# Optimization experiments

Hardware: AMD Instinct MI355X
Metric: run time of the kernel (lower is better)

## Reference

```python
import jax, jax.numpy as jnp
import numpy as np

B, N, C = 2, 8192, 64      # batch, points, feature channels
M = 2048                    # FPS-sampled centers (num_point)
KS = (16, 32)               # KNN sizes per scale
H, O = 128, 128             # EGNN hidden / output channels
S = len(KS)


def setup_inputs() -> dict:
    key = jax.random.key(0)
    k = jax.random.split(key, 12)
    sc = 0.05
    return {
        "points_xyz": jax.random.normal(k[0], (B, N, 3), jnp.float32),
        "features":   jax.random.normal(k[1], (B, C, N), jnp.float32),
        # edge MLP phi_e: [h_i, h_j, ||x_i-x_j||^2] -> H -> H
        "we1": jax.random.normal(k[2], (S, 2 * C + 1, H)) * sc,
        "be1": jnp.zeros((S, H)),
        "we2": jax.random.normal(k[3], (S, H, H)) * sc,
        "be2": jnp.zeros((S, H)),
        # coord MLP phi_x: H -> 1
        "wx": jax.random.normal(k[4], (S, H, 1)) * sc,
        "bx": jnp.zeros((S, 1)),
        # node MLP phi_h: [h_i, sum_j m_ij] -> H -> O
        "wh1": jax.random.normal(k[5], (S, C + H, H)) * sc,
        "bh1": jnp.zeros((S, H)),
        "wh2": jax.random.normal(k[6], (S, H, O)) * sc,
        "bh2": jnp.zeros((S, O)),
    }


def fps(xyz, m):
    """D-FPS: farthest point sampling by Euclidean distance. xyz (B,N,3) -> idx (B,m) int32."""
    b, n, _ = xyz.shape
    start = jnp.zeros((b,), jnp.int32)
    mind0 = jnp.full((b, n), 1e10, xyz.dtype)

    def step(carry, _):
        mind, last = carry
        lxyz = jnp.take_along_axis(xyz, last[:, None, None], axis=1)  # (B,1,3)
        d = jnp.sum((xyz - lxyz) ** 2, axis=-1)                       # (B,N)
        mind = jnp.minimum(mind, d)
        nxt = jnp.argmax(mind, axis=1).astype(jnp.int32)
        return (mind, nxt), nxt

    (_, _), rest = jax.lax.scan(step, (mind0, start), None, length=m - 1)
    return jnp.concatenate([start[:, None], rest.T], axis=1)  # (B,m)


def _forward(points_xyz, features, we1, be1, we2, be2, wx, bx, wh1, bh1, wh2, bh2):
    idx = fps(points_xyz, M)                                           # (B,M)
    dsamp_xyz = jnp.take_along_axis(points_xyz, idx[:, :, None], axis=1)   # (B,M,3)
    dsamp_feat = jnp.take_along_axis(features, idx[:, None, :], axis=2)    # (B,C,M)
    h_i = dsamp_feat.transpose(0, 2, 1)                                # (B,M,C)

    # pairwise squared distances centers->all points (B,M,N)
    d2 = (jnp.sum(dsamp_xyz ** 2, -1)[:, :, None]
          + jnp.sum(points_xyz ** 2, -1)[:, None, :]
          - 2.0 * jnp.einsum('bmd,bnd->bmn', dsamp_xyz, points_xyz))

    shifted, feats = [], []
    for i, k in enumerate(KS):
        _, nidx = jax.lax.top_k(-d2, k)                                # (B,M,k) KNN indices
        neigh_xyz = jax.vmap(lambda p, ii: p[ii])(points_xyz, nidx)    # (B,M,k,3)
        neigh_feat = jax.vmap(lambda f, ii: f[:, ii])(features, nidx)  # (B,C,M,k)
        h_j = neigh_feat.transpose(0, 2, 3, 1)                         # (B,M,k,C)

        rel = dsamp_xyz[:, :, None, :] - neigh_xyz                     # (B,M,k,3)
        dist2 = jnp.sum(rel * rel, -1, keepdims=True)                  # (B,M,k,1)

        e_in = jnp.concatenate(
            [jnp.broadcast_to(h_i[:, :, None, :], h_j.shape), h_j, dist2], axis=-1)
        m_ij = jax.nn.silu(e_in @ we1[i] + be1[i])
        m_ij = jax.nn.silu(m_ij @ we2[i] + be2[i])                     # (B,M,k,H)

        coef = m_ij @ wx[i] + bx[i]                                    # (B,M,k,1)
        x_shift = dsamp_xyz + jnp.mean(rel * coef, axis=2)             # (B,M,3)

        agg = jnp.sum(m_ij, axis=2)                                    # (B,M,H)
        h_out = jax.nn.silu(jnp.concatenate([h_i, agg], -1) @ wh1[i] + bh1[i]) @ wh2[i] + bh2[i]

        shifted.append(x_shift)
        feats.append(h_out.transpose(0, 2, 1))                         # (B,O,M)

    return (dsamp_xyz,
            jnp.concatenate(shifted, axis=1),    # (B, S*M, 3)
            jnp.concatenate(feats, axis=1),      # (B, S*O, M)
            idx)


def reference(points_xyz, features, we1, be1, we2, be2, wx, bx, wh1, bh1, wh2, bh2):
    return _forward(points_xyz, features, we1, be1, we2, be2, wx, bx, wh1, bh1, wh2, bh2)
```

## Files before the change

kernel.cpp:

```cpp
#include <hip/hip_runtime.h>
#include <stdint.h>
#include <math.h>

#define NPTS  8192
#define NB    2
#define NC    64
#define MCENT 2048
#define HH    128
#define K2NN  32

#define OUT0_OFF 0
#define OUT1_OFF (NB*MCENT*3)
#define OUT2_OFF (OUT1_OFF + NB*2*MCENT*3)
#define OUT3_OFF (OUT2_OFF + NB*2*HH*MCENT)

__device__ __forceinline__ float silu_f(float v){ return v / (1.0f + expf(-v)); }

template<int CTRL>
__device__ __forceinline__ unsigned dppmov(unsigned v){
  return (unsigned)__builtin_amdgcn_update_dpp(0, (int)v, CTRL, 0xF, 0xF, true);
}
__device__ __forceinline__ unsigned wave_max_u32(unsigned v){
  unsigned s;
  s = dppmov<0xB1>(v);  v = v > s ? v : s;
  s = dppmov<0x4E>(v);  v = v > s ? v : s;
  s = dppmov<0x141>(v); v = v > s ? v : s;
  s = dppmov<0x140>(v); v = v > s ? v : s;
  s = (unsigned)__builtin_amdgcn_ds_swizzle((int)v, 0x401F); v = v > s ? v : s;
  s = (unsigned)__shfl_xor((int)v, 32); v = v > s ? v : s;
  return v;
}
__device__ __forceinline__ unsigned wave_min_u32(unsigned v){
  unsigned s;
  s = dppmov<0xB1>(v);  v = v < s ? v : s;
  s = dppmov<0x4E>(v);  v = v < s ? v : s;
  s = dppmov<0x141>(v); v = v < s ? v : s;
  s = dppmov<0x140>(v); v = v < s ? v : s;
  s = (unsigned)__builtin_amdgcn_ds_swizzle((int)v, 0x401F); v = v < s ? v : s;
  s = (unsigned)__shfl_xor((int)v, 32); v = v < s ? v : s;
  return v;
}

__global__ __launch_bounds__(512, 2) void fps_kernel(const float* __restrict__ xyz,
                                                     float* __restrict__ out,
                                                     int* __restrict__ ws_idx){
#pragma clang fp contract(off)
  __shared__ float xs[NPTS], ys[NPTS], zs[NPTS];
  __shared__ unsigned long long warr[2][8];
  const int b   = blockIdx.x;
  const int tid = threadIdx.x;
  const float* P = xyz + (size_t)b * NPTS * 3;

  float x[16], y[16], z[16], mind[16];
  #pragma unroll
  for (int j = 0; j < 16; ++j){
    const int p = tid*16 + j;
    const float px = P[p*3+0], py = P[p*3+1], pz = P[p*3+2];
    x[j] = px; y[j] = py; z[j] = pz; mind[j] = 1e10f;
    xs[p] = px; ys[p] = py; zs[p] = pz;
  }
  float cx = P[0], cy = P[1], cz = P[2];
  if (tid == 0){
    ws_idx[b*MCENT] = 0;
    out[OUT3_OFF + b*MCENT] = 0.0f;
    out[OUT0_OFF + (size_t)(b*MCENT)*3 + 0] = cx;
    out[OUT0_OFF + (size_t)(b*MCENT)*3 + 1] = cy;
    out[OUT0_OFF + (size_t)(b*MCENT)*3 + 2] = cz;
  }
  __syncthreads();

  for (int t = 1; t < MCENT; ++t){
    float bestv = -1.0f; int bestp = tid*16;
    #pragma unroll
    for (int j = 0; j < 16; ++j){
      const float dx = x[j]-cx, dy = y[j]-cy, dz = z[j]-cz;
      const float d  = (dx*dx + dy*dy) + dz*dz;
      const float mn = fminf(mind[j], d);
      mind[j] = mn;
      if (mn > bestv){ bestv = mn; bestp = tid*16 + j; }
    }
    const unsigned vb = __float_as_uint(bestv);
    const unsigned wv = wave_max_u32(vb);
    const unsigned long long bal = __ballot(vb == wv);
    const int lane = __ffsll(bal) - 1;
    const int wp   = __shfl(bestp, lane);
    if ((tid & 63) == 0)
      warr[t & 1][tid >> 6] = ((unsigned long long)wv << 32) | (unsigned)(NPTS-1-wp);
    __syncthreads();
    unsigned long long kb = warr[t & 1][0];
    #pragma unroll
    for (int w = 1; w < 8; ++w){
      const unsigned long long k2 = warr[t & 1][w];
      if (k2 > kb) kb = k2;
    }
    const int p = NPTS - 1 - (int)(kb & 0xFFFFFFFFULL);
    cx = xs[p]; cy = ys[p]; cz = zs[p];
    if (tid == 0){
      ws_idx[b*MCENT + t] = p;
      out[OUT3_OFF + b*MCENT + t] = (float)p;
      out[OUT0_OFF + (size_t)(b*MCENT + t)*3 + 0] = cx;
      out[OUT0_OFF + (size_t)(b*MCENT + t)*3 + 1] = cy;
      out[OUT0_OFF + (size_t)(b*MCENT + t)*3 + 2] = cz;
    }
  }
}

__global__ __launch_bounds__(256) void knn_kernel(const float* __restrict__ xyz,
                                                  const float* __restrict__ out,
                                                  int* __restrict__ ws_knn){
#pragma clang fp contract(off)
  __shared__ unsigned d2u[NPTS];
  __shared__ unsigned long long warr[2][4];
  const int blk = blockIdx.x;
  const int b = blk / MCENT, m = blk % MCENT;
  const int tid = threadIdx.x;
  const float* P = xyz + (size_t)b*NPTS*3;
  const float cx = out[OUT0_OFF + (size_t)(b*MCENT+m)*3 + 0];
  const float cy = out[OUT0_OFF + (size_t)(b*MCENT+m)*3 + 1];
  const float cz = out[OUT0_OFF + (size_t)(b*MCENT+m)*3 + 2];
  const float cn = (cx*cx + cy*cy) + cz*cz;

  unsigned long long best = ~0ULL, second = ~0ULL;
  #pragma unroll 4
  for (int j = 0; j < NPTS/256; ++j){
    const int p = tid + 256*j;
    const float px = P[p*3+0], py = P[p*3+1], pz = P[p*3+2];
    const float pn = (px*px + py*py) + pz*pz;
    const float e  = (cx*px + cy*py) + cz*pz;
    const float d2 = (cn + pn) - 2.0f*e;
    unsigned u = __float_as_uint(d2);
    u = (u & 0x80000000u) ? ~u : (u | 0x80000000u);
    d2u[p] = u;
    const unsigned long long kk = ((unsigned long long)u << 32) | (unsigned)p;
    if      (kk < best)  { second = best; best = kk; }
    else if (kk < second){ second = kk; }
  }
  __syncthreads();

  for (int it = 0; it < K2NN; ++it){
    const unsigned vb = (unsigned)(best >> 32);
    const unsigned wv = wave_min_u32(vb);
    const unsigned long long bal = __ballot(vb == wv);
    unsigned long long k;
    if (__popcll(bal) == 1){
      const int lane = __ffsll(bal) - 1;
      const unsigned lp = (unsigned)__shfl((int)(unsigned)best, lane);
      k = ((unsigned long long)wv << 32) | lp;
    } else {
      k = best;
      #pragma unroll
      for (int o = 32; o > 0; o >>= 1){
        const unsigned long long k2 = __shfl_xor(k, o);
        if (k2 < k) k = k2;
      }
    }
    if ((tid & 63) == 0) warr[it & 1][tid >> 6] = k;
    __syncthreads();
    unsigned long long kb = warr[it & 1][0];
    #pragma unroll
    for (int w = 1; w < 4; ++w){
      const unsigned long long k2 = warr[it & 1][w];
      if (k2 < kb) kb = k2;
    }
    const unsigned p = (unsigned)kb;
    if (tid == 0) ws_knn[(size_t)blk*K2NN + it] = (int)p;
    if (best == kb){
      d2u[p] = 0xFFFFFFFFu;
      best = second; second = ~0ULL;
      if (best == ~0ULL){
        #pragma unroll 4
        for (int j = 0; j < NPTS/256; ++j){
          const int q = tid + 256*j;
          const unsigned long long kk = ((unsigned long long)d2u[q] << 32) | (unsigned)q;
          if      (kk < best)  { second = best; best = kk; }
          else if (kk < second){ second = kk; }
        }
      }
    }
  }
}

#define S1STR 132

template<int KNB>
__device__ __forceinline__ void egnn_scale(
    int isc, int b, int m, int tid,
    const float* __restrict__ we1, const float* __restrict__ be1,
    const float* __restrict__ we2, const float* __restrict__ be2,
    const float* __restrict__ wxw, const float* __restrict__ bxw,
    const float* __restrict__ wh1, const float* __restrict__ bh1,
    const float* __restrict__ wh2, const float* __restrict__ bh2,
    const float* hi, const float (*hj)[NC], const float (*rel)[3],
    const float* d2s, float (*s1)[S1STR], float (*s2)[S1STR],
    float* coefs, float* aggs, float* t1,
    float cx, float cy, float cz, float* __restrict__ out)
{
  constexpr int KH = KNB/2;
  const int h  = tid & 127;
  const int jg = tid >> 7;
  const int j0 = jg * KH;
  const float* W1 = we1 + (size_t)isc*129*HH;
  const float* W2 = we2 + (size_t)isc*HH*HH;

  float shi = be1[isc*HH + h];
  for (int r = 0; r < NC; ++r) shi += hi[r] * W1[r*HH + h];
  float acc[KH];
  #pragma unroll
  for (int jl = 0; jl < KH; ++jl) acc[jl] = shi;
  for (int r4 = 0; r4 < NC/4; ++r4){
    const float w0 = W1[(NC + 4*r4+0)*HH + h];
    const float w1 = W1[(NC + 4*r4+1)*HH + h];
    const float w2 = W1[(NC + 4*r4+2)*HH + h];
    const float w3 = W1[(NC + 4*r4+3)*HH + h];
    #pragma unroll
    for (int jl = 0; jl < KH; ++jl){
      const float4 v = *(const float4*)&hj[j0+jl][4*r4];
      acc[jl] += v.x*w0; acc[jl] += v.y*w1; acc[jl] += v.z*w2; acc[jl] += v.w*w3;
    }
  }
  {
    const float wd = W1[128*HH + h];
    #pragma unroll
    for (int jl = 0; jl < KH; ++jl)
      s1[j0+jl][h] = silu_f(acc[jl] + d2s[j0+jl]*wd);
  }
  __syncthreads();

  float acc2[KH];
  {
    const float b2 = be2[isc*HH + h];
    #pragma unroll
    for (int jl = 0; jl < KH; ++jl) acc2[jl] = b2;
  }
  for (int r4 = 0; r4 < HH/4; ++r4){
    const float w0 = W2[(4*r4+0)*HH + h];
    const float w1 = W2[(4*r4+1)*HH + h];
    const float w2 = W2[(4*r4+2)*HH + h];
    const float w3 = W2[(4*r4+3)*HH + h];
    #pragma unroll
    for (int jl = 0; jl < KH; ++jl){
      const float4 v = *(const float4*)&s1[j0+jl][4*r4];
      acc2[jl] += v.x*w0; acc2[jl] += v.y*w1; acc2[jl] += v.z*w2; acc2[jl] += v.w*w3;
    }
  }
  #pragma unroll
  for (int jl = 0; jl < KH; ++jl)
    s2[j0+jl][h] = silu_f(acc2[jl]);
  __syncthreads();

  if (tid < HH){
    float a = 0.f;
    #pragma unroll
    for (int j = 0; j < KNB; ++j) a += s2[j][tid];
    aggs[tid] = a;
  } else if (tid < HH + KNB){
    const int j = tid - HH;
    const float* WX = wxw + isc*HH;
    float c = 0.f;
    for (int r = 0; r < HH; ++r) c += s2[j][r]*WX[r];
    coefs[j] = c + bxw[isc];
  }
  __syncthreads();

  if (tid < 3){
    float s = 0.f;
    #pragma unroll
    for (int j = 0; j < KNB; ++j) s += rel[j][tid]*coefs[j];
    const float cc = (tid==0) ? cx : ((tid==1) ? cy : cz);
    out[OUT1_OFF + ((size_t)(b*2 + isc)*MCENT + m)*3 + tid] = cc + s*(1.0f/KNB);
  }

  if (tid < HH){
    const float* WH1 = wh1 + (size_t)isc*(NC+HH)*HH;
    float n = bh1[isc*HH + tid];
    for (int r = 0; r < NC; ++r) n += hi[r]*WH1[r*HH + tid];
    for (int r = 0; r < HH; ++r) n += aggs[r]*WH1[(NC+r)*HH + tid];
    t1[tid] = silu_f(n);
  }
  __syncthreads();

  if (tid < HH){
    const float* WH2 = wh2 + (size_t)isc*HH*HH;
    float v = bh2[isc*HH + tid];
    for (int r = 0; r < HH; ++r) v += t1[r]*WH2[r*HH + tid];
    out[OUT2_OFF + ((size_t)(b*2*HH) + isc*HH + tid)*MCENT + m] = v;
  }
  __syncthreads();
}

__global__ __launch_bounds__(256) void egnn_kernel(
    const float* __restrict__ xyz,  const float* __restrict__ feat,
    const float* __restrict__ we1,  const float* __restrict__ be1,
    const float* __restrict__ we2,  const float* __restrict__ be2,
    const float* __restrict__ wxw,  const float* __restrict__ bxw,
    const float* __restrict__ wh1,  const float* __restrict__ bh1,
    const float* __restrict__ wh2,  const float* __restrict__ bh2,
    const int* __restrict__ ws_idx, const int* __restrict__ ws_knn,
    float* __restrict__ out)
{
  __shared__ __align__(16) float hi[NC];
  __shared__ __align__(16) float hj[K2NN][NC];
  __shared__ float rel[K2NN][3];
  __shared__ float d2s[K2NN];
  __shared__ __align__(16) float s1[K2NN][S1STR];
  __shared__ __align__(16) float s2[K2NN][S1STR];
  __shared__ float coefs[K2NN];
  __shared__ float aggs[HH];
  __shared__ float t1[HH];
  __shared__ int   nidx[K2NN];

  const int blk = blockIdx.x;
  const int b = blk / MCENT, m = blk % MCENT;
  const int tid = threadIdx.x;
  const float* P = xyz + (size_t)b*NPTS*3;
  const float cx = out[OUT0_OFF + (size_t)(b*MCENT+m)*3 + 0];
  const float cy = out[OUT0_OFF + (size_t)(b*MCENT+m)*3 + 1];
  const float cz = out[OUT0_OFF + (size_t)(b*MCENT+m)*3 + 2];

  const int ci = ws_idx[b*MCENT + m];
  if (tid < NC)   hi[tid]   = feat[((size_t)b*NC + tid)*NPTS + ci];
  if (tid < K2NN) nidx[tid] = ws_knn[(size_t)blk*K2NN + tid];
  __syncthreads();

  if (tid < K2NN){
    const int p = nidx[tid];
    const float rx = cx - P[p*3+0];
    const float ry = cy - P[p*3+1];
    const float rz = cz - P[p*3+2];
    rel[tid][0]=rx; rel[tid][1]=ry; rel[tid][2]=rz;
    d2s[tid] = rx*rx + ry*ry + rz*rz;
  }
  {
    const int j  = tid >> 3;
    const int c0 = (tid & 7) * 8;
    const int p  = nidx[j];
    #pragma unroll
    for (int q = 0; q < 8; ++q)
      hj[j][c0+q] = feat[((size_t)b*NC + c0 + q)*NPTS + p];
  }
  __syncthreads();

  egnn_scale<16>(0, b, m, tid, we1, be1, we2, be2, wxw, bxw, wh1, bh1, wh2, bh2,
                 hi, hj, rel, d2s, s1, s2, coefs, aggs, t1, cx, cy, cz, out);
  egnn_scale<32>(1, b, m, tid, we1, be1, we2, be2, wxw, bxw, wh1, bh1, wh2, bh2,
                 hi, hj, rel, d2s, s1, s2, coefs, aggs, t1, cx, cy, cz, out);
}

extern "C" void kernel_launch(void* const* d_in, const int* in_sizes, int n_in,
                              void* d_out, int out_size, void* d_ws, size_t ws_size,
                              hipStream_t stream){
  const float* xyz = (const float*)d_in[0];
  const float* feat= (const float*)d_in[1];
  const float* we1 = (const float*)d_in[2];
  const float* be1 = (const float*)d_in[3];
  const float* we2 = (const float*)d_in[4];
  const float* be2 = (const float*)d_in[5];
  const float* wxw = (const float*)d_in[6];
  const float* bxw = (const float*)d_in[7];
  const float* wh1 = (const float*)d_in[8];
  const float* bh1 = (const float*)d_in[9];
  const float* wh2 = (const float*)d_in[10];
  const float* bh2 = (const float*)d_in[11];
  float* out = (float*)d_out;

  int* ws_idx = (int*)d_ws;
  int* ws_knn = ws_idx + NB*MCENT;

  fps_kernel <<<dim3(NB),        dim3(512), 0, stream>>>(xyz, out, ws_idx);
  knn_kernel <<<dim3(NB*MCENT),  dim3(256), 0, stream>>>(xyz, out, ws_knn);
  egnn_kernel<<<dim3(NB*MCENT),  dim3(256), 0, stream>>>(xyz, feat,
      we1, be1, we2, be2, wxw, bxw, wh1, bh1, wh2, bh2, ws_idx, ws_knn, out);
}
```

Before: 2.388 ms.

## Fuse FPS, KNN and EGNN into one persistent kernel with progress flags

```diff
diff --git a/kernel.cpp b/kernel.cpp
--- a/kernel.cpp
+++ b/kernel.cpp
@@ -8,27 +8,38 @@
 #define MCENT 2048
 #define HH    128
 #define K2NN  32
+#define S1STR 132
+#define GRID  256
+#define PUBMASK 7
 
 #define OUT0_OFF 0
 #define OUT1_OFF (NB*MCENT*3)
 #define OUT2_OFF (OUT1_OFF + NB*2*MCENT*3)
 #define OUT3_OFF (OUT2_OFF + NB*2*HH*MCENT)
 
+#define SM_SIZE  98432
+#define SM_XS    0
+#define SM_YS    32768
+#define SM_ZS    65536
+#define SM_FWARR 98304
+#define SM_D2U   0
+#define SM_S1    0
+#define SM_S2    16896
+#define SM_HJ    33792
+#define SM_HI    41984
+#define SM_REL   42240
+#define SM_D2S   42624
+#define SM_AGG   42752
+#define SM_T1    43264
+#define SM_COEF  43776
+#define SM_NIDX  43904
+#define SM_CWARR 44032
+
 __device__ __forceinline__ float silu_f(float v){ return v / (1.0f + expf(-v)); }
 
 template<int CTRL>
 __device__ __forceinline__ unsigned dppmov(unsigned v){
   return (unsigned)__builtin_amdgcn_update_dpp(0, (int)v, CTRL, 0xF, 0xF, true);
-}
-__device__ __forceinline__ unsigned wave_max_u32(unsigned v){
-  unsigned s;
-  s = dppmov<0xB1>(v);  v = v > s ? v : s;
-  s = dppmov<0x4E>(v);  v = v > s ? v : s;
-  s = dppmov<0x141>(v); v = v > s ? v : s;
-  s = dppmov<0x140>(v); v = v > s ? v : s;
-  s = (unsigned)__builtin_amdgcn_ds_swizzle((int)v, 0x401F); v = v > s ? v : s;
-  s = (unsigned)__shfl_xor((int)v, 32); v = v > s ? v : s;
-  return v;
 }
 __device__ __forceinline__ unsigned wave_min_u32(unsigned v){
   unsigned s;
@@ -41,14 +52,18 @@
   return v;
 }
 
-__global__ __launch_bounds__(512, 2) void fps_kernel(const float* __restrict__ xyz,
-                                                     float* __restrict__ out,
-                                                     int* __restrict__ ws_idx){
+__device__ void fps_block(const int b, const int tid,
+                          const float* __restrict__ xyz,
+                          float* __restrict__ out,
+                          int* __restrict__ ws_idx,
+                          int* __restrict__ prog,
+                          char* smem)
+{
 #pragma clang fp contract(off)
-  __shared__ float xs[NPTS], ys[NPTS], zs[NPTS];
-  __shared__ unsigned long long warr[2][8];
-  const int b   = blockIdx.x;
-  const int tid = threadIdx.x;
+  float* xs = (float*)(smem + SM_XS);
+  float* ys = (float*)(smem + SM_YS);
+  float* zs = (float*)(smem + SM_ZS);
+  unsigned long long (*warr)[8] = (unsigned long long (*)[8])(smem + SM_FWARR);
   const float* P = xyz + (size_t)b * NPTS * 3;
 
   float x[16], y[16], z[16], mind[16];
@@ -56,16 +71,16 @@
   for (int j = 0; j < 16; ++j){
     const int p = tid*16 + j;
     const float px = P[p*3+0], py = P[p*3+1], pz = P[p*3+2];
-    x[j] = px; y[j] = py; z[j] = pz; mind[j] = 1e10f;
-    xs[p] = px; ys[p] = py; zs[p] = pz;
+    x[j]=px; y[j]=py; z[j]=pz; mind[j]=1e10f;
+    xs[p]=px; ys[p]=py; zs[p]=pz;
   }
   float cx = P[0], cy = P[1], cz = P[2];
   if (tid == 0){
     ws_idx[b*MCENT] = 0;
     out[OUT3_OFF + b*MCENT] = 0.0f;
-    out[OUT0_OFF + (size_t)(b*MCENT)*3 + 0] = cx;
-    out[OUT0_OFF + (size_t)(b*MCENT)*3 + 1] = cy;
-    out[OUT0_OFF + (size_t)(b*MCENT)*3 + 2] = cz;
+    out[OUT0_OFF + (size_t)(b*MCENT)*3+0] = cx;
+    out[OUT0_OFF + (size_t)(b*MCENT)*3+1] = cy;
+    out[OUT0_OFF + (size_t)(b*MCENT)*3+2] = cz;
   }
   __syncthreads();
 
@@ -79,13 +94,14 @@
       mind[j] = mn;
       if (mn > bestv){ bestv = mn; bestp = tid*16 + j; }
     }
-    const unsigned vb = __float_as_uint(bestv);
-    const unsigned wv = wave_max_u32(vb);
-    const unsigned long long bal = __ballot(vb == wv);
-    const int lane = __ffsll(bal) - 1;
-    const int wp   = __shfl(bestp, lane);
-    if ((tid & 63) == 0)
-      warr[t & 1][tid >> 6] = ((unsigned long long)wv << 32) | (unsigned)(NPTS-1-wp);
+    unsigned long long key = ((unsigned long long)__float_as_uint(bestv) << 32)
+                           | (unsigned)(NPTS - 1 - bestp);
+    #pragma unroll
+    for (int o = 32; o > 0; o >>= 1){
+      const unsigned long long k2 = __shfl_xor(key, o);
+      if (k2 > key) key = k2;
+    }
+    if ((tid & 63) == 0) warr[t & 1][tid >> 6] = key;
     __syncthreads();
     unsigned long long kb = warr[t & 1][0];
     #pragma unroll
@@ -98,54 +114,56 @@
     if (tid == 0){
       ws_idx[b*MCENT + t] = p;
       out[OUT3_OFF + b*MCENT + t] = (float)p;
-      out[OUT0_OFF + (size_t)(b*MCENT + t)*3 + 0] = cx;
-      out[OUT0_OFF + (size_t)(b*MCENT + t)*3 + 1] = cy;
-      out[OUT0_OFF + (size_t)(b*MCENT + t)*3 + 2] = cz;
-    }
-  }
-}
-
-__global__ __launch_bounds__(256) void knn_kernel(const float* __restrict__ xyz,
-                                                  const float* __restrict__ out,
-                                                  int* __restrict__ ws_knn){
+      out[OUT0_OFF + (size_t)(b*MCENT+t)*3+0] = cx;
+      out[OUT0_OFF + (size_t)(b*MCENT+t)*3+1] = cy;
+      out[OUT0_OFF + (size_t)(b*MCENT+t)*3+2] = cz;
+      if (((t+1) & PUBMASK) == 0)
+        __hip_atomic_store(&prog[b*64], t+1, __ATOMIC_RELEASE, __HIP_MEMORY_SCOPE_AGENT);
+    }
+  }
+}
+
+__device__ void knn512(const int b, const int m, const int tid,
+                       const float* __restrict__ xyz,
+                       const float* __restrict__ out,
+                       char* smem)
+{
 #pragma clang fp contract(off)
-  __shared__ unsigned d2u[NPTS];
-  __shared__ unsigned long long warr[2][4];
-  const int blk = blockIdx.x;
-  const int b = blk / MCENT, m = blk % MCENT;
-  const int tid = threadIdx.x;
+  unsigned* d2u = (unsigned*)(smem + SM_D2U);
+  unsigned long long (*warr)[8] = (unsigned long long (*)[8])(smem + SM_CWARR);
+  int* nidx = (int*)(smem + SM_NIDX);
   const float* P = xyz + (size_t)b*NPTS*3;
-  const float cx = out[OUT0_OFF + (size_t)(b*MCENT+m)*3 + 0];
-  const float cy = out[OUT0_OFF + (size_t)(b*MCENT+m)*3 + 1];
-  const float cz = out[OUT0_OFF + (size_t)(b*MCENT+m)*3 + 2];
+  const float cx = out[OUT0_OFF + (size_t)(b*MCENT+m)*3+0];
+  const float cy = out[OUT0_OFF + (size_t)(b*MCENT+m)*3+1];
+  const float cz = out[OUT0_OFF + (size_t)(b*MCENT+m)*3+2];
   const float cn = (cx*cx + cy*cy) + cz*cz;
 
-  unsigned long long best = ~0ULL, second = ~0ULL;
+  unsigned long long best=~0ULL, second=~0ULL;
   #pragma unroll 4
-  for (int j = 0; j < NPTS/256; ++j){
-    const int p = tid + 256*j;
-    const float px = P[p*3+0], py = P[p*3+1], pz = P[p*3+2];
-    const float pn = (px*px + py*py) + pz*pz;
-    const float e  = (cx*px + cy*py) + cz*pz;
-    const float d2 = (cn + pn) - 2.0f*e;
+  for (int j = 0; j < NPTS/512; ++j){
+    const int p = tid + 512*j;
+    const float px=P[p*3+0], py=P[p*3+1], pz=P[p*3+2];
+    const float pn=(px*px+py*py)+pz*pz;
+    const float e =(cx*px+cy*py)+cz*pz;
+    const float d2=(cn+pn)-2.0f*e;
     unsigned u = __float_as_uint(d2);
     u = (u & 0x80000000u) ? ~u : (u | 0x80000000u);
     d2u[p] = u;
-    const unsigned long long kk = ((unsigned long long)u << 32) | (unsigned)p;
-    if      (kk < best)  { second = best; best = kk; }
+    const unsigned long long kk = ((unsigned long long)u<<32) | (unsigned)p;
+    if (kk < best){ second = best; best = kk; }
     else if (kk < second){ second = kk; }
   }
   __syncthreads();
 
   for (int it = 0; it < K2NN; ++it){
-    const unsigned vb = (unsigned)(best >> 32);
+    const unsigned vb = (unsigned)(best>>32);
     const unsigned wv = wave_min_u32(vb);
     const unsigned long long bal = __ballot(vb == wv);
     unsigned long long k;
     if (__popcll(bal) == 1){
-      const int lane = __ffsll(bal) - 1;
+      const int lane = __ffsll(bal)-1;
       const unsigned lp = (unsigned)__shfl((int)(unsigned)best, lane);
-      k = ((unsigned long long)wv << 32) | lp;
+      k = ((unsigned long long)wv<<32) | lp;
     } else {
       k = best;
       #pragma unroll
@@ -156,62 +174,59 @@
     }
     if ((tid & 63) == 0) warr[it & 1][tid >> 6] = k;
     __syncthreads();
-    unsigned long long kb = warr[it & 1][0];
-    #pragma unroll
-    for (int w = 1; w < 4; ++w){
-      const unsigned long long k2 = warr[it & 1][w];
+    unsigned long long kb = warr[it & 1][tid & 7];
+    #pragma unroll
+    for (int o = 4; o > 0; o >>= 1){
+      const unsigned long long k2 = __shfl_xor(kb, o);
       if (k2 < kb) kb = k2;
     }
     const unsigned p = (unsigned)kb;
-    if (tid == 0) ws_knn[(size_t)blk*K2NN + it] = (int)p;
+    if (tid == 0) nidx[it] = (int)p;
     if (best == kb){
       d2u[p] = 0xFFFFFFFFu;
       best = second; second = ~0ULL;
       if (best == ~0ULL){
         #pragma unroll 4
-        for (int j = 0; j < NPTS/256; ++j){
-          const int q = tid + 256*j;
-          const unsigned long long kk = ((unsigned long long)d2u[q] << 32) | (unsigned)q;
-          if      (kk < best)  { second = best; best = kk; }
+        for (int j = 0; j < NPTS/512; ++j){
+          const int q = tid + 512*j;
+          const unsigned long long kk = ((unsigned long long)d2u[q]<<32)|(unsigned)q;
+          if (kk < best){ second = best; best = kk; }
           else if (kk < second){ second = kk; }
         }
       }
     }
   }
-}
-
-#define S1STR 132
+  __syncthreads();
+}
 
 template<int KNB>
-__device__ __forceinline__ void egnn_scale(
-    int isc, int b, int m, int tid,
+__device__ void egnn_scale512(const int isc, const int b, const int m, const int tid,
     const float* __restrict__ we1, const float* __restrict__ be1,
     const float* __restrict__ we2, const float* __restrict__ be2,
     const float* __restrict__ wxw, const float* __restrict__ bxw,
     const float* __restrict__ wh1, const float* __restrict__ bh1,
     const float* __restrict__ wh2, const float* __restrict__ bh2,
-    const float* hi, const float (*hj)[NC], const float (*rel)[3],
-    const float* d2s, float (*s1)[S1STR], float (*s2)[S1STR],
-    float* coefs, float* aggs, float* t1,
-    float cx, float cy, float cz, float* __restrict__ out)
+    const float* hi, const float (*hj)[NC], const float (*rel)[3], const float* d2s,
+    float (*s1)[S1STR], float (*s2)[S1STR], float* coefs, float* aggs, float* t1,
+    const float cx, const float cy, const float cz, float* __restrict__ out)
 {
-  constexpr int KH = KNB/2;
+  constexpr int KH = KNB/4;
   const int h  = tid & 127;
   const int jg = tid >> 7;
   const int j0 = jg * KH;
-  const float* W1 = we1 + (size_t)isc*129*HH;
+  const float* W1 = we1 + (size_t)isc*(2*NC+1)*HH;
   const float* W2 = we2 + (size_t)isc*HH*HH;
 
   float shi = be1[isc*HH + h];
-  for (int r = 0; r < NC; ++r) shi += hi[r] * W1[r*HH + h];
+  for (int r = 0; r < NC; ++r) shi += hi[r]*W1[r*HH + h];
   float acc[KH];
   #pragma unroll
   for (int jl = 0; jl < KH; ++jl) acc[jl] = shi;
   for (int r4 = 0; r4 < NC/4; ++r4){
-    const float w0 = W1[(NC + 4*r4+0)*HH + h];
-    const float w1 = W1[(NC + 4*r4+1)*HH + h];
-    const float w2 = W1[(NC + 4*r4+2)*HH + h];
-    const float w3 = W1[(NC + 4*r4+3)*HH + h];
+    const float w0 = W1[(NC+4*r4+0)*HH+h];
+    const float w1 = W1[(NC+4*r4+1)*HH+h];
+    const float w2 = W1[(NC+4*r4+2)*HH+h];
+    const float w3 = W1[(NC+4*r4+3)*HH+h];
     #pragma unroll
     for (int jl = 0; jl < KH; ++jl){
       const float4 v = *(const float4*)&hj[j0+jl][4*r4];
@@ -219,7 +234,7 @@
     }
   }
   {
-    const float wd = W1[128*HH + h];
+    const float wd = W1[2*NC*HH + h];
     #pragma unroll
     for (int jl = 0; jl < KH; ++jl)
       s1[j0+jl][h] = silu_f(acc[jl] + d2s[j0+jl]*wd);
@@ -227,25 +242,22 @@
   __syncthreads();
 
   float acc2[KH];
-  {
-    const float b2 = be2[isc*HH + h];
-    #pragma unroll
-    for (int jl = 0; jl < KH; ++jl) acc2[jl] = b2;
-  }
+  { const float b2 = be2[isc*HH+h];
+    #pragma unroll
+    for (int jl=0;jl<KH;++jl) acc2[jl]=b2; }
   for (int r4 = 0; r4 < HH/4; ++r4){
-    const float w0 = W2[(4*r4+0)*HH + h];
-    const float w1 = W2[(4*r4+1)*HH + h];
-    const float w2 = W2[(4*r4+2)*HH + h];
-    const float w3 = W2[(4*r4+3)*HH + h];
-    #pragma unroll
-    for (int jl = 0; jl < KH; ++jl){
+    const float w0 = W2[(4*r4+0)*HH+h];
+    const float w1 = W2[(4*r4+1)*HH+h];
+    const float w2 = W2[(4*r4+2)*HH+h];
+    const float w3 = W2[(4*r4+3)*HH+h];
+    #pragma unroll
+    for (int jl=0;jl<KH;++jl){
       const float4 v = *(const float4*)&s1[j0+jl][4*r4];
-      acc2[jl] += v.x*w0; acc2[jl] += v.y*w1; acc2[jl] += v.z*w2; acc2[jl] += v.w*w3;
+      acc2[jl]+=v.x*w0; acc2[jl]+=v.y*w1; acc2[jl]+=v.z*w2; acc2[jl]+=v.w*w3;
     }
   }
   #pragma unroll
-  for (int jl = 0; jl < KH; ++jl)
-    s2[j0+jl][h] = silu_f(acc2[jl]);
+  for (int jl=0;jl<KH;++jl) s2[j0+jl][h] = silu_f(acc2[jl]);
   __syncthreads();
 
   if (tid < HH){
@@ -266,84 +278,119 @@
     float s = 0.f;
     #pragma unroll
     for (int j = 0; j < KNB; ++j) s += rel[j][tid]*coefs[j];
-    const float cc = (tid==0) ? cx : ((tid==1) ? cy : cz);
-    out[OUT1_OFF + ((size_t)(b*2 + isc)*MCENT + m)*3 + tid] = cc + s*(1.0f/KNB);
-  }
-
+    const float cc = (tid==0)?cx:((tid==1)?cy:cz);
+    out[OUT1_OFF + ((size_t)(b*2+isc)*MCENT + m)*3 + tid] = cc + s*(1.0f/KNB);
+  }
   if (tid < HH){
     const float* WH1 = wh1 + (size_t)isc*(NC+HH)*HH;
     float n = bh1[isc*HH + tid];
-    for (int r = 0; r < NC; ++r) n += hi[r]*WH1[r*HH + tid];
-    for (int r = 0; r < HH; ++r) n += aggs[r]*WH1[(NC+r)*HH + tid];
+    for (int r = 0; r < NC; ++r) n += hi[r]*WH1[r*HH+tid];
+    for (int r = 0; r < HH; ++r) n += aggs[r]*WH1[(NC+r)*HH+tid];
     t1[tid] = silu_f(n);
   }
   __syncthreads();
-
   if (tid < HH){
     const float* WH2 = wh2 + (size_t)isc*HH*HH;
     float v = bh2[isc*HH + tid];
-    for (int r = 0; r < HH; ++r) v += t1[r]*WH2[r*HH + tid];
+    for (int r = 0; r < HH; ++r) v += t1[r]*WH2[r*HH+tid];
     out[OUT2_OFF + ((size_t)(b*2*HH) + isc*HH + tid)*MCENT + m] = v;
   }
   __syncthreads();
 }
 
-__global__ __launch_bounds__(256) void egnn_kernel(
-    const float* __restrict__ xyz,  const float* __restrict__ feat,
-    const float* __restrict__ we1,  const float* __restrict__ be1,
-    const float* __restrict__ we2,  const float* __restrict__ be2,
-    const float* __restrict__ wxw,  const float* __restrict__ bxw,
-    const float* __restrict__ wh1,  const float* __restrict__ bh1,
-    const float* __restrict__ wh2,  const float* __restrict__ bh2,
-    const int* __restrict__ ws_idx, const int* __restrict__ ws_knn,
+__device__ void consumer_block(const int tid,
+    const float* __restrict__ xyz, const float* __restrict__ feat,
+    const float* __restrict__ we1, const float* __restrict__ be1,
+    const float* __restrict__ we2, const float* __restrict__ be2,
+    const float* __restrict__ wxw, const float* __restrict__ bxw,
+    const float* __restrict__ wh1, const float* __restrict__ bh1,
+    const float* __restrict__ wh2, const float* __restrict__ bh2,
+    const int* __restrict__ ws_idx, int* __restrict__ prog,
+    float* __restrict__ out, char* smem)
+{
+  float (*s1)[S1STR] = (float (*)[S1STR])(smem + SM_S1);
+  float (*s2)[S1STR] = (float (*)[S1STR])(smem + SM_S2);
+  float (*hj)[NC]    = (float (*)[NC])(smem + SM_HJ);
+  float* hi    = (float*)(smem + SM_HI);
+  float (*rel)[3] = (float (*)[3])(smem + SM_REL);
+  float* d2s   = (float*)(smem + SM_D2S);
+  float* aggs  = (float*)(smem + SM_AGG);
+  float* t1    = (float*)(smem + SM_T1);
+  float* coefs = (float*)(smem + SM_COEF);
+  int* nidx    = (int*)(smem + SM_NIDX);
+
+  const int nitems = NB*MCENT;
+  for (int item = (int)blockIdx.x - NB; item < nitems; item += (int)gridDim.x - NB){
+    const int b = item >> 11;
+    const int m = item & (MCENT-1);
+    if (tid == 0){
+      long spins = 0;
+      for (;;){
+        const int pv = __hip_atomic_load(&prog[b*64], __ATOMIC_ACQUIRE,
+                                         __HIP_MEMORY_SCOPE_AGENT);
+        if (pv >= m+1) break;
+        if (m+1-pv > 64) __builtin_amdgcn_s_sleep(64);
+        else             __builtin_amdgcn_s_sleep(4);
+        if (++spins > 60000000L) break;
+      }
+    }
+    __syncthreads();
+
+    knn512(b, m, tid, xyz, out, smem);
+
+    const float* P = xyz + (size_t)b*NPTS*3;
+    const float cx = out[OUT0_OFF + (size_t)(b*MCENT+m)*3+0];
+    const float cy = out[OUT0_OFF + (size_t)(b*MCENT+m)*3+1];
+    const float cz = out[OUT0_OFF + (size_t)(b*MCENT+m)*3+2];
+    const int ci = ws_idx[b*MCENT + m];
+    if (tid < NC) hi[tid] = feat[((size_t)b*NC + tid)*NPTS + ci];
+    if (tid < K2NN){
+      const int p = nidx[tid];
+      const float rx = cx - P[p*3+0];
+      const float ry = cy - P[p*3+1];
+      const float rz = cz - P[p*3+2];
+      rel[tid][0]=rx; rel[tid][1]=ry; rel[tid][2]=rz;
+      d2s[tid] = rx*rx + ry*ry + rz*rz;
+    }
+    {
+      const int j  = tid >> 4;
+      const int c0 = (tid & 15) * 4;
+      const int p  = nidx[j];
+      #pragma unroll
+      for (int q = 0; q < 4; ++q)
+        hj[j][c0+q] = feat[((size_t)b*NC + c0 + q)*NPTS + p];
+    }
+    __syncthreads();
+
+    egnn_scale512<16>(0, b, m, tid, we1,be1,we2,be2,wxw,bxw,wh1,bh1,wh2,bh2,
+                      hi, hj, rel, d2s, s1, s2, coefs, aggs, t1, cx, cy, cz, out);
+    egnn_scale512<32>(1, b, m, tid, we1,be1,we2,be2,wxw,bxw,wh1,bh1,wh2,bh2,
+                      hi, hj, rel, d2s, s1, s2, coefs, aggs, t1, cx, cy, cz, out);
+  }
+}
+
+__global__ __launch_bounds__(512, 2) void fused_kernel(
+    const float* __restrict__ xyz, const float* __restrict__ feat,
+    const float* __restrict__ we1, const float* __restrict__ be1,
+    const float* __restrict__ we2, const float* __restrict__ be2,
+    const float* __restrict__ wxw, const float* __restrict__ bxw,
+    const float* __restrict__ wh1, const float* __restrict__ bh1,
+    const float* __restrict__ wh2, const float* __restrict__ bh2,
+    int* __restrict__ ws_idx, int* __restrict__ prog,
     float* __restrict__ out)
 {
-  __shared__ __align__(16) float hi[NC];
-  __shared__ __align__(16) float hj[K2NN][NC];
-  __shared__ float rel[K2NN][3];
-  __shared__ float d2s[K2NN];
-  __shared__ __align__(16) float s1[K2NN][S1STR];
-  __shared__ __align__(16) float s2[K2NN][S1STR];
-  __shared__ float coefs[K2NN];
-  __shared__ float aggs[HH];
-  __shared__ float t1[HH];
-  __shared__ int   nidx[K2NN];
-
-  const int blk = blockIdx.x;
-  const int b = blk / MCENT, m = blk % MCENT;
+  __shared__ __align__(16) char smem[SM_SIZE];
   const int tid = threadIdx.x;
-  const float* P = xyz + (size_t)b*NPTS*3;
-  const float cx = out[OUT0_OFF + (size_t)(b*MCENT+m)*3 + 0];
-  const float cy = out[OUT0_OFF + (size_t)(b*MCENT+m)*3 + 1];
-  const float cz = out[OUT0_OFF + (size_t)(b*MCENT+m)*3 + 2];
-
-  const int ci = ws_idx[b*MCENT + m];
-  if (tid < NC)   hi[tid]   = feat[((size_t)b*NC + tid)*NPTS + ci];
-  if (tid < K2NN) nidx[tid] = ws_knn[(size_t)blk*K2NN + tid];
-  __syncthreads();
-
-  if (tid < K2NN){
-    const int p = nidx[tid];
-    const float rx = cx - P[p*3+0];
-    const float ry = cy - P[p*3+1];
-    const float rz = cz - P[p*3+2];
-    rel[tid][0]=rx; rel[tid][1]=ry; rel[tid][2]=rz;
-    d2s[tid] = rx*rx + ry*ry + rz*rz;
-  }
-  {
-    const int j  = tid >> 3;
-    const int c0 = (tid & 7) * 8;
-    const int p  = nidx[j];
-    #pragma unroll
-    for (int q = 0; q < 8; ++q)
-      hj[j][c0+q] = feat[((size_t)b*NC + c0 + q)*NPTS + p];
-  }
-  __syncthreads();
-
-  egnn_scale<16>(0, b, m, tid, we1, be1, we2, be2, wxw, bxw, wh1, bh1, wh2, bh2,
-                 hi, hj, rel, d2s, s1, s2, coefs, aggs, t1, cx, cy, cz, out);
-  egnn_scale<32>(1, b, m, tid, we1, be1, we2, be2, wxw, bxw, wh1, bh1, wh2, bh2,
-                 hi, hj, rel, d2s, s1, s2, coefs, aggs, t1, cx, cy, cz, out);
+  if (blockIdx.x < NB){
+    fps_block((int)blockIdx.x, tid, xyz, out, ws_idx, prog, smem);
+  } else {
+    consumer_block(tid, xyz, feat, we1,be1,we2,be2,wxw,bxw,wh1,bh1,wh2,bh2,
+                   ws_idx, prog, out, smem);
+  }
+}
+
+__global__ void init_kernel(int* __restrict__ prog){
+  prog[threadIdx.x] = 0;
 }
 
 extern "C" void kernel_launch(void* const* d_in, const int* in_sizes, int n_in,
@@ -363,11 +410,10 @@
   const float* bh2 = (const float*)d_in[11];
   float* out = (float*)d_out;
 
-  int* ws_idx = (int*)d_ws;
-  int* ws_knn = ws_idx + NB*MCENT;
-
-  fps_kernel <<<dim3(NB),        dim3(512), 0, stream>>>(xyz, out, ws_idx);
-  knn_kernel <<<dim3(NB*MCENT),  dim3(256), 0, stream>>>(xyz, out, ws_knn);
-  egnn_kernel<<<dim3(NB*MCENT),  dim3(256), 0, stream>>>(xyz, feat,
-      we1, be1, we2, be2, wxw, bxw, wh1, bh1, wh2, bh2, ws_idx, ws_knn, out);
-}
+  int* prog   = (int*)d_ws;
+  int* ws_idx = prog + 128;
+
+  init_kernel <<<dim3(1),    dim3(128), 0, stream>>>(prog);
+  fused_kernel<<<dim3(GRID), dim3(512), 0, stream>>>(xyz, feat,
+      we1, be1, we2, be2, wxw, bxw, wh1, bh1, wh2, bh2, ws_idx, prog, out);
+}
```

New measurement: 4.697 ms. 96.7% more time.

## Prune FPS distance updates with spatially sorted point groups and bounding spheres

Applied to the files above, without the earlier changes.

```diff
diff --git a/kernel.cpp b/kernel.cpp
--- a/kernel.cpp
+++ b/kernel.cpp
@@ -8,11 +8,28 @@
 #define MCENT 2048
 #define HH    128
 #define K2NN  32
+#define NCELL 4096
+
+typedef unsigned long long ull;
 
 #define OUT0_OFF 0
 #define OUT1_OFF (NB*MCENT*3)
 #define OUT2_OFF (OUT1_OFF + NB*2*MCENT*3)
 #define OUT3_OFF (OUT2_OFF + NB*2*HH*MCENT)
+
+#define F_SX    0
+#define F_SY    32768
+#define F_SZ    65536
+#define F_MIND  98304
+#define F_CNT   98304
+#define F_OFF   114688
+#define F_SORIG 131072
+#define F_GK    147456
+#define F_LIST  151552
+#define F_WARR  152576
+#define F_PART  152704
+#define F_NLIST 154752
+#define F_SIZE  154816
 
 __device__ __forceinline__ float silu_f(float v){ return v / (1.0f + expf(-v)); }
 
@@ -41,26 +58,84 @@
   return v;
 }
 
-__global__ __launch_bounds__(512, 2) void fps_kernel(const float* __restrict__ xyz,
+__device__ __forceinline__ void bar_lds(){
+  asm volatile("s_waitcnt lgkmcnt(0)" ::: "memory");
+  __builtin_amdgcn_s_barrier();
+}
+
+__global__ __launch_bounds__(512, 1) void fps_kernel(const float* __restrict__ xyz,
                                                      float* __restrict__ out,
                                                      int* __restrict__ ws_idx){
 #pragma clang fp contract(off)
-  __shared__ float xs[NPTS], ys[NPTS], zs[NPTS];
-  __shared__ unsigned long long warr[2][8];
+  __shared__ __align__(16) char smem[F_SIZE];
+  float* sx   = (float*)(smem + F_SX);
+  float* sy   = (float*)(smem + F_SY);
+  float* sz   = (float*)(smem + F_SZ);
+  float* mind = (float*)(smem + F_MIND);
+  int*   cnt  = (int*)(smem + F_CNT);
+  int*   off  = (int*)(smem + F_OFF);
+  unsigned short* sorig = (unsigned short*)(smem + F_SORIG);
+  ull*   gk   = (ull*)(smem + F_GK);
+  unsigned short* list  = (unsigned short*)(smem + F_LIST);
+  ull (*warr)[8] = (ull (*)[8])(smem + F_WARR);
+  int*   part = (int*)(smem + F_PART);
+  int*   nlist= (int*)(smem + F_NLIST);
+
   const int b   = blockIdx.x;
   const int tid = threadIdx.x;
+  const int lane = tid & 63, wid = tid >> 6;
   const float* P = xyz + (size_t)b * NPTS * 3;
 
-  float x[16], y[16], z[16], mind[16];
+  float lx[16], ly[16], lz[16]; int lc[16];
+  for (int i = tid; i < NCELL; i += 512) cnt[i] = 0;
+  __syncthreads();
   #pragma unroll
   for (int j = 0; j < 16; ++j){
     const int p = tid*16 + j;
-    const float px = P[p*3+0], py = P[p*3+1], pz = P[p*3+2];
-    x[j] = px; y[j] = py; z[j] = pz; mind[j] = 1e10f;
-    xs[p] = px; ys[p] = py; zs[p] = pz;
-  }
+    const float x = P[p*3+0], y = P[p*3+1], z = P[p*3+2];
+    lx[j]=x; ly[j]=y; lz[j]=z;
+    int ix = (int)floorf((x + 5.0f) * 1.6f); ix = ix<0?0:(ix>15?15:ix);
+    int iy = (int)floorf((y + 5.0f) * 1.6f); iy = iy<0?0:(iy>15?15:iy);
+    int iz = (int)floorf((z + 5.0f) * 1.6f); iz = iz<0?0:(iz>15?15:iz);
+    lc[j] = (ix<<8)|(iy<<4)|iz;
+    atomicAdd(&cnt[lc[j]], 1);
+  }
+  __syncthreads();
+  { int s = 0;
+    #pragma unroll
+    for (int k = 0; k < 8; ++k) s += cnt[tid*8+k];
+    part[tid] = s; }
+  __syncthreads();
+  if (tid == 0){ int run = 0;
+    for (int i = 0; i < 512; ++i){ const int v = part[i]; part[i] = run; run += v; } }
+  __syncthreads();
+  { int bse = part[tid];
+    #pragma unroll
+    for (int k = 0; k < 8; ++k){ off[tid*8+k] = bse; bse += cnt[tid*8+k]; } }
+  __syncthreads();
+  #pragma unroll
+  for (int j = 0; j < 16; ++j){
+    const int pos = atomicAdd(&off[lc[j]], 1);
+    sx[pos]=lx[j]; sy[pos]=ly[j]; sz[pos]=lz[j];
+    sorig[pos] = (unsigned short)(tid*16 + j);
+  }
+  __syncthreads();
+  float gcx=0.f, gcy=0.f, gcz=0.f;
+  #pragma unroll
+  for (int j = 0; j < 16; ++j){ gcx += sx[tid*16+j]; gcy += sy[tid*16+j]; gcz += sz[tid*16+j]; }
+  gcx *= 0.0625f; gcy *= 0.0625f; gcz *= 0.0625f;
+  float r2 = 0.f;
+  #pragma unroll
+  for (int j = 0; j < 16; ++j){
+    const float dx = sx[tid*16+j]-gcx, dy = sy[tid*16+j]-gcy, dz = sz[tid*16+j]-gcz;
+    r2 = fmaxf(r2, dx*dx + dy*dy + dz*dz);
+  }
+  const float gr = sqrtf(r2)*1.0005f + 1e-5f;
+  for (int i = tid; i < NPTS; i += 512) mind[i] = 1e10f;
+  gk[tid] = ((ull)__float_as_uint(1e10f) << 32);
   float cx = P[0], cy = P[1], cz = P[2];
   if (tid == 0){
+    *nlist = 0;
     ws_idx[b*MCENT] = 0;
     out[OUT3_OFF + b*MCENT] = 0.0f;
     out[OUT0_OFF + (size_t)(b*MCENT)*3 + 0] = cx;
@@ -70,34 +145,69 @@
   __syncthreads();
 
   for (int t = 1; t < MCENT; ++t){
-    float bestv = -1.0f; int bestp = tid*16;
-    #pragma unroll
-    for (int j = 0; j < 16; ++j){
-      const float dx = x[j]-cx, dy = y[j]-cy, dz = z[j]-cz;
-      const float d  = (dx*dx + dy*dy) + dz*dz;
-      const float mn = fminf(mind[j], d);
-      mind[j] = mn;
-      if (mn > bestv){ bestv = mn; bestp = tid*16 + j; }
-    }
-    const unsigned vb = __float_as_uint(bestv);
-    const unsigned wv = wave_max_u32(vb);
-    const unsigned long long bal = __ballot(vb == wv);
-    const int lane = __ffsll(bal) - 1;
-    const int wp   = __shfl(bestp, lane);
-    if ((tid & 63) == 0)
-      warr[t & 1][tid >> 6] = ((unsigned long long)wv << 32) | (unsigned)(NPTS-1-wp);
-    __syncthreads();
-    unsigned long long kb = warr[t & 1][0];
-    #pragma unroll
-    for (int w = 1; w < 8; ++w){
-      const unsigned long long k2 = warr[t & 1][w];
-      if (k2 > kb) kb = k2;
-    }
-    const int p = NPTS - 1 - (int)(kb & 0xFFFFFFFFULL);
-    cx = xs[p]; cy = ys[p]; cz = zs[p];
+    const ull   myk  = gk[tid];
+    const float gmax = __uint_as_float((unsigned)(myk >> 32));
+    const float dxg = gcx-cx, dyg = gcy-cy, dzg = gcz-cz;
+    const float dg  = dxg*dxg + dyg*dyg + dzg*dzg;
+    const float lb  = sqrtf(dg)*0.99995f - gr;
+    bool touched = true;
+    if (lb > 0.0f) touched = !(lb*lb*0.9999f > gmax);
+    const ull mask = __ballot(touched);
+    int base0 = 0;
+    if (lane == 0 && mask) base0 = atomicAdd(nlist, __popcll(mask));
+    base0 = __shfl(base0, 0);
+    if (touched){
+      const int pfx = __popcll(mask & ((1ULL << lane) - 1ULL));
+      list[base0 + pfx] = (unsigned short)tid;
+    }
+    bar_lds();
+    const int n = *nlist;
+    if (tid < n){
+      const int g  = list[tid];
+      const int sb = g << 4;
+      ull bk = 0;
+      for (int j = 0; j < 16; ++j){
+        const int sp = sb + j;
+        const float dx = sx[sp]-cx, dy = sy[sp]-cy, dz = sz[sp]-cz;
+        const float d  = (dx*dx + dy*dy) + dz*dz;
+        const float mn = fminf(mind[sp], d);
+        mind[sp] = mn;
+        const ull key = ((ull)__float_as_uint(mn) << 32)
+                      | ((ull)(unsigned)(NPTS-1-(int)sorig[sp]) << 13)
+                      | (unsigned)sp;
+        if (key > bk) bk = key;
+      }
+      gk[g] = bk;
+    }
+    bar_lds();
+    const ull k2 = gk[tid];
+    const unsigned vb = (unsigned)(k2 >> 32);
+    const unsigned wm = wave_max_u32(vb);
+    const ull balm = __ballot(vb == wm);
+    ull wkey;
+    if (__popcll(balm) == 1){
+      const int sl = __ffsll(balm) - 1;
+      wkey = __shfl(k2, sl);
+    } else {
+      wkey = k2;
+      #pragma unroll
+      for (int o = 32; o > 0; o >>= 1){
+        const ull q = __shfl_xor(wkey, o);
+        if (q > wkey) wkey = q;
+      }
+    }
+    if (lane == 0) warr[t & 1][wid] = wkey;
+    if (tid == 0) *nlist = 0;
+    bar_lds();
+    ull best = warr[t & 1][0];
+    #pragma unroll
+    for (int w = 1; w < 8; ++w){ const ull q = warr[t & 1][w]; if (q > best) best = q; }
+    const int sp    = (int)(best & 0x1FFFULL);
+    const int porig = NPTS - 1 - (int)((best >> 13) & 0x1FFFULL);
+    cx = sx[sp]; cy = sy[sp]; cz = sz[sp];
     if (tid == 0){
-      ws_idx[b*MCENT + t] = p;
-      out[OUT3_OFF + b*MCENT + t] = (float)p;
+      ws_idx[b*MCENT + t] = porig;
+      out[OUT3_OFF + b*MCENT + t] = (float)porig;
       out[OUT0_OFF + (size_t)(b*MCENT + t)*3 + 0] = cx;
       out[OUT0_OFF + (size_t)(b*MCENT + t)*3 + 1] = cy;
       out[OUT0_OFF + (size_t)(b*MCENT + t)*3 + 2] = cz;
@@ -269,7 +379,6 @@
     const float cc = (tid==0) ? cx : ((tid==1) ? cy : cz);
     out[OUT1_OFF + ((size_t)(b*2 + isc)*MCENT + m)*3 + tid] = cc + s*(1.0f/KNB);
   }
-
   if (tid < HH){
     const float* WH1 = wh1 + (size_t)isc*(NC+HH)*HH;
     float n = bh1[isc*HH + tid];
@@ -278,7 +387,6 @@
     t1[tid] = silu_f(n);
   }
   __syncthreads();
-
   if (tid < HH){
     const float* WH2 = wh2 + (size_t)isc*HH*HH;
     float v = bh2[isc*HH + tid];
@@ -366,8 +474,8 @@
   int* ws_idx = (int*)d_ws;
   int* ws_knn = ws_idx + NB*MCENT;
 
-  fps_kernel <<<dim3(NB),        dim3(512), 0, stream>>>(xyz, out, ws_idx);
-  knn_kernel <<<dim3(NB*MCENT),  dim3(256), 0, stream>>>(xyz, out, ws_knn);
-  egnn_kernel<<<dim3(NB*MCENT),  dim3(256), 0, stream>>>(xyz, feat,
+  fps_kernel <<<dim3(NB),       dim3(512), 0, stream>>>(xyz, out, ws_idx);
+  knn_kernel <<<dim3(NB*MCENT), dim3(256), 0, stream>>>(xyz, out, ws_knn);
+  egnn_kernel<<<dim3(NB*MCENT), dim3(256), 0, stream>>>(xyz, feat,
       we1, be1, we2, be2, wxw, bxw, wh1, bh1, wh2, bh2, ws_idx, ws_knn, out);
 }
```

After: 4.304 ms. 1.8x slower.
